# Kernel tuning notes

Measured on AMD Instinct MI355X. Metric: run time of the kernel, lower is better.

The kernel has to match this reference:

```python
import jax, jax.numpy as jnp
import numpy as np

N = 20000      # nodes per side
E = 160000     # edges
C = 512        # input_channels
C_OUT = 512    # output_channels
TEMP = float(np.sqrt(C))  # self.temperature = sqrt(input_channels)
NEG_SLOPE = 0.01          # LeakyReLU default


def _xavier(key, shape):
    fan_in, fan_out = shape[1], shape[0]
    std = np.sqrt(2.0 / (fan_in + fan_out))
    return jax.random.normal(key, shape, dtype=jnp.float32) * std


def setup_inputs() -> dict:
    key = jax.random.key(0)
    ks = jax.random.split(key, 10)
    return {
        "node_left": jax.random.normal(ks[0], (N, C), dtype=jnp.float32),
        "segmentation_index_left": jax.random.randint(ks[1], (E,), 0, N),
        "index_left": jax.random.randint(ks[2], (E,), 0, N),
        "node_right": jax.random.normal(ks[3], (N, C), dtype=jnp.float32),
        "segmentation_index_right": jax.random.randint(ks[4], (E,), 0, N),
        "index_right": jax.random.randint(ks[5], (E,), 0, N),
        "Wk": _xavier(ks[6], (C, C)),      # key_projection.weight
        "Wv": _xavier(ks[7], (C, C)),      # value_projection.weight
        "Wo": _xavier(ks[8], (C_OUT, C)),  # out_projection Linear weight
        "bo": jnp.zeros((C_OUT,), dtype=jnp.float32),
    }


def segment_softmax(scores, seg_idx, num_segments, temperature):
    # numerically stable softmax over variable-length segments of edges
    s = scores / temperature
    m = jax.ops.segment_max(s, seg_idx, num_segments=num_segments)
    m = jnp.where(jnp.isneginf(m), 0.0, m)  # guard empty segments
    e = jnp.exp(s - m[seg_idx])
    z = jax.ops.segment_sum(e, seg_idx, num_segments=num_segments)
    return e / z[seg_idx]


def _message(translation, seg_idx, num_segments, neighbor, Wo, bo):
    attn = segment_softmax(translation, seg_idx, num_segments, TEMP)  # [E]
    # dropout is identity at inference
    msg = jax.ops.segment_sum(attn[:, None] * neighbor, seg_idx,
                              num_segments=num_segments)  # [N, C]
    h = msg @ Wo.T + bo
    return jnp.where(h >= 0, h, NEG_SLOPE * h)  # LeakyReLU


def reference(node_left, segmentation_index_left, index_left,
              node_right, segmentation_index_right, index_right,
              Wk, Wv, Wo, bo):
    n_left = node_left.shape[0]
    n_right = node_right.shape[0]
    # key projections gathered to edges
    left_center = (node_left @ Wk.T)[segmentation_index_left]    # [E, C]
    right_center = (node_right @ Wk.T)[segmentation_index_right]  # [E, C]
    # value projections gathered to edges (cross side)
    left_neighbor = (node_right @ Wv.T)[segmentation_index_right]  # [E, C]
    right_neighbor = (node_left @ Wv.T)[segmentation_index_left]   # [E, C]
    translation = jnp.sum(left_center * right_center, axis=1)      # [E]
    msg_left = _message(translation, segmentation_index_left, n_left,
                        left_neighbor, Wo, bo)
    msg_right = _message(translation, segmentation_index_right, n_right,
                         right_neighbor, Wo, bo)
    return (msg_left, msg_right)
```

## Files before the change

kernel.cpp:

```cpp
#include <hip/hip_runtime.h>


#define C_DIM 512
#define TEMP_INV (1.0f / 22.627416997969522f)

using bf16x8 = __attribute__((ext_vector_type(8))) __bf16;
using s16x8  = __attribute__((ext_vector_type(8))) short;
using s16x4  = __attribute__((ext_vector_type(4))) short;
using f32x4  = __attribute__((ext_vector_type(4))) float;

__device__ __forceinline__ float bf2f(short u) {
    union { unsigned u; float f; } t;
    t.u = ((unsigned)(unsigned short)u) << 16;
    return t.f;
}
__device__ __forceinline__ short f2bf(float f) {
    union { float f; unsigned u; } t;
    t.f = f;
    unsigned r = t.u + 0x7FFFu + ((t.u >> 16) & 1u);
    return (short)(r >> 16);
}

__global__ void cvt2_f32_bf16(const float* __restrict__ inA,
                              const float* __restrict__ inB,
                              short* __restrict__ out, long n4half) {
    long i = (long)blockIdx.x * blockDim.x + threadIdx.x;
    long stride = (long)gridDim.x * blockDim.x;
    long n4 = 2 * n4half;
    for (; i < n4; i += stride) {
        const float4* src = (i < n4half)
            ? reinterpret_cast<const float4*>(inA) + i
            : reinterpret_cast<const float4*>(inB) + (i - n4half);
        float4 v = *src;
        s16x4 o;
        o[0] = f2bf(v.x); o[1] = f2bf(v.y); o[2] = f2bf(v.z); o[3] = f2bf(v.w);
        reinterpret_cast<s16x4*>(out)[i] = o;
    }
}

__global__ void cvt_weights(const float* __restrict__ Wk,
                            const float* __restrict__ Wv,
                            const float* __restrict__ Wo,
                            short* __restrict__ Wkc, short* __restrict__ WoB,
                            short* __restrict__ WvT) {
    int b = blockIdx.x;
    int tid = threadIdx.x;
    if (b < 64) {
        __shared__ float t[64][65];
        int bx = b & 7, by = b >> 3;
#pragma unroll
        for (int i = 0; i < 4; ++i) {
            int idx = i * 256 + tid;
            int row = idx >> 4, c4 = idx & 15;
            float4 v = *(const float4*)&Wv[(size_t)(by * 64 + row) * 512 + bx * 64 + c4 * 4];
            t[row][c4 * 4 + 0] = v.x; t[row][c4 * 4 + 1] = v.y;
            t[row][c4 * 4 + 2] = v.z; t[row][c4 * 4 + 3] = v.w;
        }
        __syncthreads();
#pragma unroll
        for (int i = 0; i < 4; ++i) {
            int idx = i * 256 + tid;
            int row = idx >> 4, g = idx & 15;
            s16x4 o;
            o[0] = f2bf(t[g * 4 + 0][row]);
            o[1] = f2bf(t[g * 4 + 1][row]);
            o[2] = f2bf(t[g * 4 + 2][row]);
            o[3] = f2bf(t[g * 4 + 3][row]);
            *(s16x4*)&WvT[(size_t)(bx * 64 + row) * 512 + by * 64 + g * 4] = o;
        }
    } else {
        const float* src = (b < 128) ? Wk : Wo;
        short* dst = (b < 128) ? Wkc : WoB;
        long base = (long)(b & 63) * 1024;
#pragma unroll
        for (int i = 0; i < 4; ++i) {
            long idx = base + i * 256 + tid;
            float4 v = reinterpret_cast<const float4*>(src)[idx];
            s16x4 o;
            o[0] = f2bf(v.x); o[1] = f2bf(v.y); o[2] = f2bf(v.z); o[3] = f2bf(v.w);
            reinterpret_cast<s16x4*>(dst)[idx] = o;
        }
    }
}

__global__ __launch_bounds__(256, 4)
void gemm_bt(const short* __restrict__ A, const short* __restrict__ B,
             short* __restrict__ Cp, int M, int N, int K, int nn, int total) {
    __shared__ short As[2][128 * 32];
    __shared__ short Bs[2][128 * 32];

    const int bid = blockIdx.x;
    const int q = total >> 3, r = total & 7;
    const int xcd = bid & 7, idx = bid >> 3;
    const int swz = (xcd < r ? xcd * (q + 1) : r * (q + 1) + (xcd - r) * q) + idx;
    const int bm = (swz / nn) * 128;
    const int bn = (swz % nn) * 128;

    const int tid  = threadIdx.x;
    const int lane = tid & 63;
    const int wid  = tid >> 6;
    const int wm   = (wid >> 1) * 64;
    const int wn   = (wid & 1) * 64;
    const int lrow  = lane & 15;
    const int khalf = lane >> 4;

    auto stage = [&](short* dA, short* dB, int k0) {
#pragma unroll
        for (int j = 0; j < 2; ++j) {
            int L    = j * 256 + tid;
            int pr   = L >> 3;
            int slot = L & 7;
            int g    = slot ^ (pr & 7);
            int row  = pr * 2 + (g >> 2);
            int kg   = g & 3;
            int wb   = (j * 256 + (tid & ~63)) * 16;
            {
                int grow = bm + row; if (grow >= M) grow = M - 1;
                const short* src = A + (size_t)grow * K + k0 + kg * 8;
                __builtin_amdgcn_global_load_lds(
                    (__attribute__((address_space(1))) void*)src,
                    (__attribute__((address_space(3))) void*)((char*)dA + wb),
                    16, 0, 0);
            }
            {
                int grow = bn + row; if (grow >= N) grow = N - 1;
                const short* src = B + (size_t)grow * K + k0 + kg * 8;
                __builtin_amdgcn_global_load_lds(
                    (__attribute__((address_space(1))) void*)src,
                    (__attribute__((address_space(3))) void*)((char*)dB + wb),
                    16, 0, 0);
            }
        }
    };

    auto frag = [&](const short* h, int row) -> bf16x8 {
        int pr   = row >> 1;
        int g    = ((row & 1) << 2) | khalf;
        int slot = g ^ (pr & 7);
        return *(const bf16x8*)&h[pr * 64 + slot * 8];
    };

    f32x4 acc[4][4] = {};
    const int nt = K >> 5;

    stage(As[0], Bs[0], 0);

    for (int t = 0; t < nt; ++t) {
        const int cur = t & 1;
        if (t + 1 < nt) {
            stage(As[cur ^ 1], Bs[cur ^ 1], (t + 1) << 5);
            asm volatile("s_waitcnt vmcnt(4)" ::: "memory");
        } else {
            asm volatile("s_waitcnt vmcnt(0)" ::: "memory");
        }
        __builtin_amdgcn_s_barrier();

        const short* as = As[cur];
        const short* bs = Bs[cur];
        bf16x8 af[4], bfr[4];
#pragma unroll
        for (int m = 0; m < 4; ++m) af[m] = frag(as, wm + m * 16 + lrow);
#pragma unroll
        for (int n = 0; n < 4; ++n) bfr[n] = frag(bs, wn + n * 16 + lrow);

        asm volatile("s_waitcnt lgkmcnt(0)" ::: "memory");
        __builtin_amdgcn_sched_barrier(0);
        __builtin_amdgcn_s_barrier();

        __builtin_amdgcn_s_setprio(1);
#pragma unroll
        for (int m = 0; m < 4; ++m)
#pragma unroll
            for (int n = 0; n < 4; ++n)
                acc[m][n] = __builtin_amdgcn_mfma_f32_16x16x32_bf16(
                    af[m], bfr[n], acc[m][n], 0, 0, 0);
        __builtin_amdgcn_s_setprio(0);
    }

    const int crow0 = (lane >> 4) * 4;
    const int ccol  = lane & 15;
#pragma unroll
    for (int m = 0; m < 4; ++m) {
#pragma unroll
        for (int n = 0; n < 4; ++n) {
            int col = bn + wn + n * 16 + ccol;
#pragma unroll
            for (int r2 = 0; r2 < 4; ++r2) {
                int row = bm + wm + m * 16 + crow0 + r2;
                if (row < M) Cp[(size_t)row * N + col] = f2bf(acc[m][n][r2]);
            }
        }
    }
}

__global__ void edge_dot(const short* __restrict__ proj,
                         const int* __restrict__ segL, const int* __restrict__ segR,
                         float* __restrict__ w, int* __restrict__ cnt,
                         int E, int N) {
    int e0 = blockIdx.x * 16 + (threadIdx.x >> 6) * 4;
    if (e0 >= E) return;
    int lane = threadIdx.x & 63;

    int e[4];
    float sum[4];
#pragma unroll
    for (int k = 0; k < 4; ++k) {
        int ek = e0 + k;
        e[k] = (ek < E) ? ek : e0;
        const short* a = proj + (size_t)segL[e[k]] * 1024 + lane * 8;
        const short* b = proj + (size_t)(N + segR[e[k]]) * 1024 + lane * 8;
        s16x8 va = *(const s16x8*)a;
        s16x8 vb = *(const s16x8*)b;
        float s = 0.f;
#pragma unroll
        for (int j = 0; j < 8; ++j) s += bf2f(va[j]) * bf2f(vb[j]);
        sum[k] = s;
    }
#pragma unroll
    for (int o = 32; o > 0; o >>= 1) {
#pragma unroll
        for (int k = 0; k < 4; ++k) sum[k] += __shfl_xor(sum[k], o, 64);
    }
    if (lane < 4) {
        int ek = e0 + lane;
        if (ek < E) {
            float s = (lane == 0) ? sum[0] : (lane == 1) ? sum[1]
                    : (lane == 2) ? sum[2] : sum[3];
            w[ek] = __expf(s * TEMP_INV);
            atomicAdd(&cnt[segL[ek]], 1);
            atomicAdd(&cnt[N + segR[ek]], 1);
        }
    }
}

__global__ void scan_blocks(const int* __restrict__ cnt, int* __restrict__ off,
                            int* __restrict__ bsum, int n) {
    __shared__ int ws[4];
    int tid = threadIdx.x, lane = tid & 63, wid = tid >> 6;
    int i = blockIdx.x * 256 + tid;
    int x = (i < n) ? cnt[i] : 0;
    int v = x;
#pragma unroll
    for (int d = 1; d < 64; d <<= 1) {
        int t = __shfl_up(v, d, 64);
        if (lane >= d) v += t;
    }
    if (lane == 63) ws[wid] = v;
    __syncthreads();
    int woff = 0;
    for (int w = 0; w < wid; ++w) woff += ws[w];
    v += woff;
    if (i < n) off[i + 1] = v;
    if (tid == 255) bsum[blockIdx.x] = v;
}

__global__ void scan_tops(int* __restrict__ bsum, int nb) {
    __shared__ int ws[4];
    int tid = threadIdx.x, lane = tid & 63, wid = tid >> 6;
    int x = (tid < nb) ? bsum[tid] : 0;
    int v = x;
#pragma unroll
    for (int d = 1; d < 64; d <<= 1) {
        int t = __shfl_up(v, d, 64);
        if (lane >= d) v += t;
    }
    if (lane == 63) ws[wid] = v;
    __syncthreads();
    int woff = 0;
    for (int w = 0; w < wid; ++w) woff += ws[w];
    v += woff;
    if (tid < nb) bsum[tid] = v - x;
}

__global__ void scan_apply(int* __restrict__ off, const int* __restrict__ bsum,
                           int* __restrict__ cnt, int n) {
    int i = blockIdx.x * 256 + threadIdx.x;
    if (i < n) {
        off[i + 1] += bsum[blockIdx.x];
        cnt[i] = 0;
    }
    if (i == 0) off[0] = 0;
}

__global__ void fill_csr2(const int* __restrict__ segL, const int* __restrict__ segR,
                          const float* __restrict__ w,
                          const int* __restrict__ off, int* __restrict__ cur,
                          float2* __restrict__ pairs, int E, int N) {
    int i = blockIdx.x * blockDim.x + threadIdx.x;
    int st = gridDim.x * blockDim.x;
    for (; i < E; i += st) {
        int sl = segL[i], sr = segR[i];
        float we = w[i];
        int pl = off[sl] + atomicAdd(&cur[sl], 1);
        pairs[pl] = make_float2(we, __int_as_float(N + sr));
        int pr = off[N + sr] + atomicAdd(&cur[N + sr], 1);
        pairs[pr] = make_float2(we, __int_as_float(sl));
    }
}

__global__ void node_msg(const int* __restrict__ off,
                         const float2* __restrict__ pairs,
                         const short* __restrict__ proj,
                         const float* __restrict__ bo,
                         float* __restrict__ out, int NN2) {
    int n = blockIdx.x * 4 + (threadIdx.x >> 6);
    if (n >= NN2) return;
    int lane = threadIdx.x & 63;
    int beg = off[n], end = off[n + 1];
    const short* VW = proj + 512 + lane * 8;

    float acc[8] = {};
    float z = 0.f;
    int i = beg;
    for (; i + 3 < end; i += 4) {
        float2 p0 = pairs[i], p1 = pairs[i + 1];
        float2 p2 = pairs[i + 2], p3 = pairs[i + 3];
        const s16x8 v0 = *(const s16x8*)(VW + (size_t)__float_as_int(p0.y) * 1024);
        const s16x8 v1 = *(const s16x8*)(VW + (size_t)__float_as_int(p1.y) * 1024);
        const s16x8 v2 = *(const s16x8*)(VW + (size_t)__float_as_int(p2.y) * 1024);
        const s16x8 v3 = *(const s16x8*)(VW + (size_t)__float_as_int(p3.y) * 1024);
        z += (p0.x + p1.x) + (p2.x + p3.x);
#pragma unroll
        for (int j = 0; j < 8; ++j) {
            acc[j] += p0.x * bf2f(v0[j]) + p1.x * bf2f(v1[j]);
            acc[j] += p2.x * bf2f(v2[j]) + p3.x * bf2f(v3[j]);
        }
    }
    for (; i < end; ++i) {
        float2 p = pairs[i];
        const s16x8 v = *(const s16x8*)(VW + (size_t)__float_as_int(p.y) * 1024);
        z += p.x;
#pragma unroll
        for (int j = 0; j < 8; ++j) acc[j] += p.x * bf2f(v[j]);
    }
    float inv = (z > 0.f) ? 1.f / z : 0.f;

    float4 bs0 = *(const float4*)&bo[lane * 8];
    float4 bs1 = *(const float4*)&bo[lane * 8 + 4];
    float bb[8] = {bs0.x, bs0.y, bs0.z, bs0.w, bs1.x, bs1.y, bs1.z, bs1.w};
    float h[8];
#pragma unroll
    for (int j = 0; j < 8; ++j) {
        float v = acc[j] * inv + bb[j];
        h[j] = v >= 0.f ? v : 0.01f * v;
    }
    float* orow = out + (size_t)n * C_DIM + lane * 8;
    *(float4*)&orow[0] = make_float4(h[0], h[1], h[2], h[3]);
    *(float4*)&orow[4] = make_float4(h[4], h[5], h[6], h[7]);
}

extern "C" void kernel_launch(void* const* d_in, const int* in_sizes, int n_in,
                              void* d_out, int out_size, void* d_ws, size_t ws_size,
                              hipStream_t stream) {
    const float* node_left  = (const float*)d_in[0];
    const int*   segL       = (const int*)d_in[1];
    const float* node_right = (const float*)d_in[3];
    const int*   segR       = (const int*)d_in[4];
    const float* Wk         = (const float*)d_in[6];
    const float* Wv         = (const float*)d_in[7];
    const float* Wo         = (const float*)d_in[8];
    const float* bo         = (const float*)d_in[9];

    const int C = C_DIM;
    const int N = in_sizes[0] / C;
    const int E = in_sizes[1];
    const int NN2 = 2 * N;

    size_t offb = 0;
    auto alloc = [&](size_t bytes) -> void* {
        void* p = (char*)d_ws + offb;
        offb += (bytes + 255) & ~(size_t)255;
        return p;
    };
    short* nodeLR_b = (short*)alloc((size_t)NN2 * C * 2);
    short* Wkc_b  = (short*)alloc((size_t)1024 * C * 2);
    short* Wc_b   = Wkc_b + (size_t)C * C;
    short* Wo_b   = (short*)alloc((size_t)C * C * 2);
    short* WvT_b  = (short*)alloc((size_t)C * C * 2);
    short* proj   = (short*)alloc((size_t)NN2 * 1024 * 2);
    float* w_arr  = (float*)alloc((size_t)E * 4);
    float2* pairs = (float2*)alloc((size_t)2 * E * 8);
    int* cnt  = (int*)alloc((size_t)NN2 * 4);
    int* off  = (int*)alloc((size_t)(NN2 + 1) * 4);
    int* bsum = (int*)alloc(256 * 4);

    const int nsb = (NN2 + 255) / 256;

    hipMemsetAsync(cnt, 0, (size_t)NN2 * 4, stream);
    cvt2_f32_bf16<<<2048, 256, 0, stream>>>(node_left, node_right, nodeLR_b,
                                            (long)N * C / 4);
    cvt_weights<<<192, 256, 0, stream>>>(Wk, Wv, Wo, Wkc_b, Wo_b, WvT_b);

    gemm_bt<<<16, 256, 0, stream>>>(Wo_b, WvT_b, Wc_b, C, C, C, 4, 16);
    {
        int nm = (NN2 + 127) / 128, nn = 1024 / 128;
        int total = nm * nn;
        gemm_bt<<<total, 256, 0, stream>>>(nodeLR_b, Wkc_b, proj, NN2, 1024, C,
                                           nn, total);
    }

    edge_dot<<<(E + 15) / 16, 256, 0, stream>>>(proj, segL, segR, w_arr, cnt, E, N);

    scan_blocks<<<nsb, 256, 0, stream>>>(cnt, off, bsum, NN2);
    scan_tops<<<1, 256, 0, stream>>>(bsum, nsb);
    scan_apply<<<nsb, 256, 0, stream>>>(off, bsum, cnt, NN2);
    fill_csr2<<<512, 256, 0, stream>>>(segL, segR, w_arr, off, cnt, pairs, E, N);

    node_msg<<<(NN2 + 3) / 4, 256, 0, stream>>>(off, pairs, proj, bo,
                                                (float*)d_out, NN2);
}
```

Before: 222.4 us.

## Replace 128x128 GEMM with 256x256-tile 8-wave kernel and nontemporal output stores

```diff
diff --git a/kernel.cpp b/kernel.cpp
--- a/kernel.cpp
+++ b/kernel.cpp
@@ -83,111 +83,168 @@
     }
 }
 
-__global__ __launch_bounds__(256, 4)
-void gemm_bt(const short* __restrict__ A, const short* __restrict__ B,
+
+__device__ __forceinline__ void stage_half(const short* __restrict__ mat,
+                                           int row0, int k0, int K, int M,
+                                           short* dst, int tid) {
+#pragma unroll
+    for (int j = 0; j < 2; ++j) {
+        int L    = j * 512 + tid;
+        int pr   = L >> 3;
+        int slot = L & 7;
+        int g    = slot ^ (pr & 7);
+        int gr   = row0 + pr; if (gr >= M) gr = M - 1;
+        const short* s = mat + (size_t)gr * K + k0 + g * 8;
+        int wb = (j * 512 + (tid & ~63)) * 16;
+        __builtin_amdgcn_global_load_lds(
+            (__attribute__((address_space(1))) void*)s,
+            (__attribute__((address_space(3))) void*)((char*)dst + wb),
+            16, 0, 0);
+    }
+}
+
+__global__ __launch_bounds__(512, 2)
+void gemm256(const short* __restrict__ A, const short* __restrict__ B,
              short* __restrict__ Cp, int M, int N, int K, int nn, int total) {
-    __shared__ short As[2][128 * 32];
-    __shared__ short Bs[2][128 * 32];
+    __shared__ short As[2][2][128 * 64];
+    __shared__ short Bs[2][2][128 * 64];
 
     const int bid = blockIdx.x;
     const int q = total >> 3, r = total & 7;
     const int xcd = bid & 7, idx = bid >> 3;
     const int swz = (xcd < r ? xcd * (q + 1) : r * (q + 1) + (xcd - r) * q) + idx;
-    const int bm = (swz / nn) * 128;
-    const int bn = (swz % nn) * 128;
-
-    const int tid  = threadIdx.x;
-    const int lane = tid & 63;
-    const int wid  = tid >> 6;
-    const int wm   = (wid >> 1) * 64;
-    const int wn   = (wid & 1) * 64;
+    const int bm = (swz / nn) * 256;
+    const int bn = (swz % nn) * 256;
+
+    const int tid   = threadIdx.x;
+    const int lane  = tid & 63;
+    const int wid   = tid >> 6;
+    const int wm    = wid >> 2;
+    const int wn    = wid & 3;
     const int lrow  = lane & 15;
     const int khalf = lane >> 4;
-
-    auto stage = [&](short* dA, short* dB, int k0) {
-#pragma unroll
-        for (int j = 0; j < 2; ++j) {
-            int L    = j * 256 + tid;
-            int pr   = L >> 3;
-            int slot = L & 7;
-            int g    = slot ^ (pr & 7);
-            int row  = pr * 2 + (g >> 2);
-            int kg   = g & 3;
-            int wb   = (j * 256 + (tid & ~63)) * 16;
-            {
-                int grow = bm + row; if (grow >= M) grow = M - 1;
-                const short* src = A + (size_t)grow * K + k0 + kg * 8;
-                __builtin_amdgcn_global_load_lds(
-                    (__attribute__((address_space(1))) void*)src,
-                    (__attribute__((address_space(3))) void*)((char*)dA + wb),
-                    16, 0, 0);
-            }
-            {
-                int grow = bn + row; if (grow >= N) grow = N - 1;
-                const short* src = B + (size_t)grow * K + k0 + kg * 8;
-                __builtin_amdgcn_global_load_lds(
-                    (__attribute__((address_space(1))) void*)src,
-                    (__attribute__((address_space(3))) void*)((char*)dB + wb),
-                    16, 0, 0);
-            }
-        }
-    };
-
-    auto frag = [&](const short* h, int row) -> bf16x8 {
-        int pr   = row >> 1;
-        int g    = ((row & 1) << 2) | khalf;
-        int slot = g ^ (pr & 7);
-        return *(const bf16x8*)&h[pr * 64 + slot * 8];
-    };
-
-    f32x4 acc[4][4] = {};
-    const int nt = K >> 5;
-
-    stage(As[0], Bs[0], 0);
-
-    for (int t = 0; t < nt; ++t) {
-        const int cur = t & 1;
-        if (t + 1 < nt) {
-            stage(As[cur ^ 1], Bs[cur ^ 1], (t + 1) << 5);
-            asm volatile("s_waitcnt vmcnt(4)" ::: "memory");
+    const int brow0 = (wn & 1) * 64;
+
+    f32x4 acc[8][4] = {};
+    bf16x8 a[4][2], b[4][2];
+
+    const int nt = K >> 6;
+
+    stage_half(A, bm,       0, K, M, As[0][0], tid);
+    stage_half(A, bm + 128, 0, K, M, As[0][1], tid);
+    stage_half(B, bn,       0, K, N, Bs[0][0], tid);
+    stage_half(B, bn + 128, 0, K, N, Bs[0][1], tid);
+
+    for (int kt = 0; kt < nt; ++kt) {
+        const int buf = kt & 1;
+        const short* Ah = As[buf][wm];
+        const short* Bh = Bs[buf][wn >> 1];
+        const bool pre = (kt + 1) < nt;
+        const int k1 = (kt + 1) << 6;
+
+        auto frag = [&](const short* h, int row, int ks) -> bf16x8 {
+            int g = ks * 4 + khalf;
+            int slot = g ^ (row & 7);
+            return *(const bf16x8*)&h[row * 64 + slot * 8];
+        };
+
+        if (pre) {
+            stage_half(A, bm,       k1, K, M, As[buf ^ 1][0], tid);
+            stage_half(A, bm + 128, k1, K, M, As[buf ^ 1][1], tid);
+            stage_half(B, bn,       k1, K, N, Bs[buf ^ 1][0], tid);
+            stage_half(B, bn + 128, k1, K, N, Bs[buf ^ 1][1], tid);
+            asm volatile("s_waitcnt vmcnt(8)" ::: "memory");
         } else {
             asm volatile("s_waitcnt vmcnt(0)" ::: "memory");
         }
         __builtin_amdgcn_s_barrier();
 
-        const short* as = As[cur];
-        const short* bs = Bs[cur];
-        bf16x8 af[4], bfr[4];
-#pragma unroll
-        for (int m = 0; m < 4; ++m) af[m] = frag(as, wm + m * 16 + lrow);
-#pragma unroll
-        for (int n = 0; n < 4; ++n) bfr[n] = frag(bs, wn + n * 16 + lrow);
-
+#pragma unroll
+        for (int mf = 0; mf < 4; ++mf)
+#pragma unroll
+            for (int ks = 0; ks < 2; ++ks)
+                a[mf][ks] = frag(Ah, mf * 16 + lrow, ks);
+#pragma unroll
+        for (int nf = 0; nf < 2; ++nf)
+#pragma unroll
+            for (int ks = 0; ks < 2; ++ks)
+                b[nf][ks] = frag(Bh, brow0 + nf * 16 + lrow, ks);
         asm volatile("s_waitcnt lgkmcnt(0)" ::: "memory");
         __builtin_amdgcn_sched_barrier(0);
+        __builtin_amdgcn_s_setprio(1);
+#pragma unroll
+        for (int mf = 0; mf < 4; ++mf)
+#pragma unroll
+            for (int nf = 0; nf < 2; ++nf)
+#pragma unroll
+                for (int ks = 0; ks < 2; ++ks)
+                    acc[mf][nf] = __builtin_amdgcn_mfma_f32_16x16x32_bf16(
+                        a[mf][ks], b[nf][ks], acc[mf][nf], 0, 0, 0);
+        __builtin_amdgcn_s_setprio(0);
         __builtin_amdgcn_s_barrier();
 
+#pragma unroll
+        for (int nf = 2; nf < 4; ++nf)
+#pragma unroll
+            for (int ks = 0; ks < 2; ++ks)
+                b[nf][ks] = frag(Bh, brow0 + nf * 16 + lrow, ks);
+        asm volatile("s_waitcnt lgkmcnt(0)" ::: "memory");
+        __builtin_amdgcn_sched_barrier(0);
         __builtin_amdgcn_s_setprio(1);
 #pragma unroll
-        for (int m = 0; m < 4; ++m)
-#pragma unroll
-            for (int n = 0; n < 4; ++n)
-                acc[m][n] = __builtin_amdgcn_mfma_f32_16x16x32_bf16(
-                    af[m], bfr[n], acc[m][n], 0, 0, 0);
+        for (int mf = 0; mf < 4; ++mf)
+#pragma unroll
+            for (int nf = 2; nf < 4; ++nf)
+#pragma unroll
+                for (int ks = 0; ks < 2; ++ks)
+                    acc[mf][nf] = __builtin_amdgcn_mfma_f32_16x16x32_bf16(
+                        a[mf][ks], b[nf][ks], acc[mf][nf], 0, 0, 0);
         __builtin_amdgcn_s_setprio(0);
+        __builtin_amdgcn_s_barrier();
+
+#pragma unroll
+        for (int mf = 0; mf < 4; ++mf)
+#pragma unroll
+            for (int ks = 0; ks < 2; ++ks)
+                a[mf][ks] = frag(Ah, 64 + mf * 16 + lrow, ks);
+        asm volatile("s_waitcnt lgkmcnt(0)" ::: "memory");
+        __builtin_amdgcn_sched_barrier(0);
+        __builtin_amdgcn_s_setprio(1);
+#pragma unroll
+        for (int mf = 0; mf < 4; ++mf)
+#pragma unroll
+            for (int nf = 0; nf < 2; ++nf)
+#pragma unroll
+                for (int ks = 0; ks < 2; ++ks)
+                    acc[4 + mf][nf] = __builtin_amdgcn_mfma_f32_16x16x32_bf16(
+                        a[mf][ks], b[nf][ks], acc[4 + mf][nf], 0, 0, 0);
+        __builtin_amdgcn_s_setprio(0);
+        __builtin_amdgcn_s_barrier();
+
+        __builtin_amdgcn_s_setprio(1);
+#pragma unroll
+        for (int mf = 0; mf < 4; ++mf)
+#pragma unroll
+            for (int nf = 2; nf < 4; ++nf)
+#pragma unroll
+                for (int ks = 0; ks < 2; ++ks)
+                    acc[4 + mf][nf] = __builtin_amdgcn_mfma_f32_16x16x32_bf16(
+                        a[mf][ks], b[nf][ks], acc[4 + mf][nf], 0, 0, 0);
+        __builtin_amdgcn_s_setprio(0);
+        __builtin_amdgcn_s_barrier();
     }
 
     const int crow0 = (lane >> 4) * 4;
     const int ccol  = lane & 15;
 #pragma unroll
-    for (int m = 0; m < 4; ++m) {
-#pragma unroll
-        for (int n = 0; n < 4; ++n) {
-            int col = bn + wn + n * 16 + ccol;
+    for (int qf = 0; qf < 8; ++qf) {
+#pragma unroll
+        for (int nf = 0; nf < 4; ++nf) {
+            int col = bn + wn * 64 + nf * 16 + ccol;
 #pragma unroll
             for (int r2 = 0; r2 < 4; ++r2) {
-                int row = bm + wm + m * 16 + crow0 + r2;
-                if (row < M) Cp[(size_t)row * N + col] = f2bf(acc[m][n][r2]);
+                int row = bm + wm * 128 + qf * 16 + crow0 + r2;
+                if (row < M) Cp[(size_t)row * N + col] = f2bf(acc[qf][nf][r2]);
             }
         }
     }
@@ -338,15 +395,20 @@
     float4 bs0 = *(const float4*)&bo[lane * 8];
     float4 bs1 = *(const float4*)&bo[lane * 8 + 4];
     float bb[8] = {bs0.x, bs0.y, bs0.z, bs0.w, bs1.x, bs1.y, bs1.z, bs1.w};
-    float h[8];
-#pragma unroll
-    for (int j = 0; j < 8; ++j) {
+    f32x4 h0, h1;
+#pragma unroll
+    for (int j = 0; j < 4; ++j) {
         float v = acc[j] * inv + bb[j];
-        h[j] = v >= 0.f ? v : 0.01f * v;
+        h0[j] = v >= 0.f ? v : 0.01f * v;
+    }
+#pragma unroll
+    for (int j = 0; j < 4; ++j) {
+        float v = acc[4 + j] * inv + bb[4 + j];
+        h1[j] = v >= 0.f ? v : 0.01f * v;
     }
     float* orow = out + (size_t)n * C_DIM + lane * 8;
-    *(float4*)&orow[0] = make_float4(h[0], h[1], h[2], h[3]);
-    *(float4*)&orow[4] = make_float4(h[4], h[5], h[6], h[7]);
+    __builtin_nontemporal_store(h0, (f32x4*)&orow[0]);
+    __builtin_nontemporal_store(h1, (f32x4*)&orow[4]);
 }
 
 extern "C" void kernel_launch(void* const* d_in, const int* in_sizes, int n_in,
@@ -391,11 +453,11 @@
                                             (long)N * C / 4);
     cvt_weights<<<192, 256, 0, stream>>>(Wk, Wv, Wo, Wkc_b, Wo_b, WvT_b);
 
-    gemm_bt<<<16, 256, 0, stream>>>(Wo_b, WvT_b, Wc_b, C, C, C, 4, 16);
+    gemm256<<<4, 512, 0, stream>>>(Wo_b, WvT_b, Wc_b, C, C, C, 2, 4);
     {
-        int nm = (NN2 + 127) / 128, nn = 1024 / 128;
+        int nm = (NN2 + 255) / 256, nn = 1024 / 256;
         int total = nm * nn;
-        gemm_bt<<<total, 256, 0, stream>>>(nodeLR_b, Wkc_b, proj, NN2, 1024, C,
+        gemm256<<<total, 512, 0, stream>>>(nodeLR_b, Wkc_b, proj, NN2, 1024, C,
                                            nn, total);
     }
 
```

Result: slower. 238.0 us (+7.0%).
